# Kernel tuning notes

Measured on AMD Instinct MI355X. Metric: run time of the kernel, lower is better.

The kernel has to match this reference:

```python
import jax, jax.numpy as jnp
import numpy as np
from jax import lax

OUT = 24
THRESHOLD = 0.7
IOU_THRESHOLD = 0.5


def _conv(x, w, b):
    # x: [N,C,H,W], w: [O,I,kh,kw] (torch OIHW), valid padding, stride 1
    y = lax.conv_general_dilated(x, w, (1, 1), 'VALID',
                                 dimension_numbers=('NCHW', 'OIHW', 'NCHW'))
    return y + b[None, :, None, None]


def _prelu(x, a):
    a = a.reshape((1, -1) + (1,) * (x.ndim - 2))
    return jnp.where(x > 0, x, a * x)


def _maxpool(x, k, s, p):
    return lax.reduce_window(x, -jnp.inf, lax.max,
                             (1, 1, k, k), (1, 1, s, s),
                             [(0, 0), (0, 0), (p, p), (p, p)])


def _crop_resize(img, bboxes):
    # img: [3,H,W]; nearest-neighbor resize of each (clipped) crop to 24x24,
    # matching F.interpolate default nearest mode: src = floor(dst*in/out).
    _, H, W = img.shape
    x1 = jnp.clip(bboxes[:, 0].astype(jnp.int32), 0, W)
    y1 = jnp.clip(bboxes[:, 1].astype(jnp.int32), 0, H)
    x2 = jnp.clip(bboxes[:, 2].astype(jnp.int32), 0, W)
    y2 = jnp.clip(bboxes[:, 3].astype(jnp.int32), 0, H)
    j = jnp.arange(OUT)
    ix = jnp.clip(x1[:, None] + (j[None, :] * (x2 - x1)[:, None]) // OUT, 0, W - 1)  # [N,24]
    iy = jnp.clip(y1[:, None] + (j[None, :] * (y2 - y1)[:, None]) // OUT, 0, H - 1)  # [N,24]
    crops = img[:, iy[:, :, None], ix[:, None, :]]  # [3,N,24,24]
    return jnp.transpose(crops, (1, 0, 2, 3))        # [N,3,24,24]


def _pairwise_iou(b):
    x1 = jnp.maximum(b[:, None, 0], b[None, :, 0])
    y1 = jnp.maximum(b[:, None, 1], b[None, :, 1])
    x2 = jnp.minimum(b[:, None, 2], b[None, :, 2])
    y2 = jnp.minimum(b[:, None, 3], b[None, :, 3])
    inter = jnp.clip(x2 - x1, 0) * jnp.clip(y2 - y1, 0)
    area = jnp.clip(b[:, 2] - b[:, 0], 0) * jnp.clip(b[:, 3] - b[:, 1], 0)
    return inter / jnp.maximum(area[:, None] + area[None, :] - inter, 1e-12)


def _nms_keep(boxes, scores, valid, iou_thr):
    # Fixed-shape greedy NMS: returns boolean keep mask over original order.
    N = boxes.shape[0]
    order = jnp.argsort(-scores)
    b = boxes[order]
    v = valid[order]
    iou = _pairwise_iou(b)
    idx = jnp.arange(N)

    def body(i, supp):
        alive = v[i] & jnp.logical_not(supp[i])
        kill = alive & (iou[i] > iou_thr) & (idx > i)
        return supp | kill

    supp = lax.fori_loop(0, N, body, jnp.zeros((N,), bool))
    keep_sorted = v & jnp.logical_not(supp)
    return jnp.zeros((N,), bool).at[order].set(keep_sorted)


def _forward(image, bboxes, conv1_w, conv1_b, prelu1_a, conv2_w, conv2_b, prelu2_a,
             conv3_w, conv3_b, prelu3_a, lin4_w, lin4_b, prelu4_a,
             lin5a_w, lin5a_b, lin5b_w, lin5b_b):
    img = jnp.transpose((image - 127.5) * 0.0078125, (2, 0, 1))  # preprocess, HWC->CHW
    x = _crop_resize(img, bboxes)                                 # [N,3,24,24]
    x = _maxpool(_prelu(_conv(x, conv1_w, conv1_b), prelu1_a), 3, 2, 1)   # [N,28,11,11]
    x = _maxpool(_prelu(_conv(x, conv2_w, conv2_b), prelu2_a), 3, 2, 0)   # [N,48,4,4]
    x = _prelu(_conv(x, conv3_w, conv3_b), prelu3_a)                      # [N,64,3,3]
    x = x.reshape(x.shape[0], -1)                                          # [N,576]
    x = _prelu(x @ lin4_w.T + lin4_b, prelu4_a)                            # [N,128]
    cls = jax.nn.softmax(x @ lin5a_w.T + lin5a_b, axis=1)
    reg = x @ lin5b_w.T + lin5b_b
    scores = cls[:, 1]
    w = bboxes[:, 2] - bboxes[:, 0]
    h = bboxes[:, 3] - bboxes[:, 1]
    boxes = jnp.stack([bboxes[:, 0] + reg[:, 0] * w,
                       bboxes[:, 1] + reg[:, 1] * h,
                       bboxes[:, 2] + reg[:, 2] * w,
                       bboxes[:, 3] + reg[:, 3] * h], axis=1)
    return boxes, scores


def setup_inputs() -> dict:
    key = jax.random.key(0)
    ks = jax.random.split(key, 20)
    H, W, N = 1080, 1920, 4096
    image = jax.random.uniform(ks[0], (H, W, 3), jnp.float32, 0.0, 255.0)
    x1 = jax.random.randint(ks[1], (N,), 0, W - 96).astype(jnp.float32)
    y1 = jax.random.randint(ks[2], (N,), 0, H - 96).astype(jnp.float32)
    bw = jax.random.randint(ks[3], (N,), 24, 96).astype(jnp.float32)
    bh = jax.random.randint(ks[4], (N,), 24, 96).astype(jnp.float32)
    bboxes = jnp.stack([x1, y1, x1 + bw, y1 + bh], axis=1)

    def w(k, shape, scale):
        return jax.random.normal(k, shape, jnp.float32) * scale

    return dict(
        image=image, bboxes=bboxes,
        conv1_w=w(ks[5], (28, 3, 3, 3), 0.1), conv1_b=w(ks[6], (28,), 0.01),
        prelu1_a=jnp.full((28,), 0.25, jnp.float32),
        conv2_w=w(ks[7], (48, 28, 3, 3), 0.06), conv2_b=w(ks[8], (48,), 0.01),
        prelu2_a=jnp.full((48,), 0.25, jnp.float32),
        conv3_w=w(ks[9], (64, 48, 2, 2), 0.07), conv3_b=w(ks[10], (64,), 0.01),
        prelu3_a=jnp.full((64,), 0.25, jnp.float32),
        lin4_w=w(ks[11], (128, 576), 0.04), lin4_b=w(ks[12], (128,), 0.01),
        prelu4_a=jnp.full((128,), 0.25, jnp.float32),
        lin5a_w=w(ks[13], (2, 128), 0.2), lin5a_b=w(ks[14], (2,), 0.01),
        lin5b_w=w(ks[15], (4, 128), 0.09), lin5b_b=w(ks[16], (4,), 0.01),
    )


def reference(image, bboxes, conv1_w, conv1_b, prelu1_a, conv2_w, conv2_b, prelu2_a,
              conv3_w, conv3_b, prelu3_a, lin4_w, lin4_b, prelu4_a,
              lin5a_w, lin5a_b, lin5b_w, lin5b_b):
    boxes, scores = _forward(image, bboxes, conv1_w, conv1_b, prelu1_a,
                             conv2_w, conv2_b, prelu2_a, conv3_w, conv3_b, prelu3_a,
                             lin4_w, lin4_b, prelu4_a, lin5a_w, lin5a_b, lin5b_w, lin5b_b)
    valid = scores >= THRESHOLD
    keep = _nms_keep(boxes, scores, valid, IOU_THRESHOLD)
    # padded (masked) form of `bboxes[pick, :]` so output shape is static
    return jnp.where(keep[:, None], boxes, 0.0)
```

## Files before the change

kernel.cpp:

```cpp
#include <hip/hip_runtime.h>

typedef unsigned long long ull;
typedef __attribute__((ext_vector_type(8))) short bf16x8;
typedef __attribute__((ext_vector_type(4))) float f32x4;

#define W_IMG 1920
#define H_IMG 1080
#define NBOX 4096

#define S_CROP   0
#define S_CBUF   2016
#define S_PLANES 5152
#define S_BUF2   0
#define S_POOL2  3888
#define S_FEAT   0
#define S_VEC    576
#define S_LOUT   704
#define SMEM_F   8848

#define WS_BT    2277392
#define WS_BT1   2332688

__device__ __forceinline__ float4 ld4(const float* p) { return *(const float4*)p; }
__device__ __forceinline__ float prelu_f(float v, float a) { return v > 0.f ? v : a * v; }
__device__ __forceinline__ unsigned short bf16rn(float v) {
  unsigned u = __float_as_uint(v);
  return (unsigned short)((u + 0x7fffu + ((u >> 16) & 1u)) >> 16);
}
__device__ __forceinline__ float bf16tof(unsigned short h) {
  return __uint_as_float(((unsigned)h) << 16);
}

__global__ __launch_bounds__(256) void wconv_kernel(const float* __restrict__ w2,
                                                    const float* __restrict__ w1,
                                                    unsigned short* __restrict__ bt,
                                                    unsigned short* __restrict__ bt1) {
  int b = blockIdx.x, tid = threadIdx.x;
  if (b < 16) {
    for (int e = b*864 + tid; e < (b+1)*864; e += 256) {
      int c = e & 31, rest = e >> 5;
      int co = rest % 48, kk = rest / 48;
      float v = (c < 28) ? w2[co*252 + c*9 + kk] : 0.f;
      unsigned short h1 = bf16rn(v);
      bt[e] = h1;
      bt[13824 + e] = bf16rn(v - bf16tof(h1));
    }
  } else {
    for (int e = tid; e < 2048; e += 256) {
      int j = e & 7, rest = e >> 3;
      int co = rest & 31, pg = rest >> 5;
      int grp = pg & 3, plane = pg >> 2;
      int k = grp*8 + j;
      float v = (k < 27 && co < 28) ? w1[co*27 + k] : 0.f;
      unsigned short h1 = bf16rn(v);
      bt1[e] = plane ? bf16rn(v - bf16tof(h1)) : h1;
    }
  }
}

__global__ __launch_bounds__(256, 4) void cnn_kernel(
    const float* __restrict__ image, const float* __restrict__ bboxes,
    const unsigned short* __restrict__ wbt1,
    const float* __restrict__ b1, const float* __restrict__ a1,
    const unsigned short* __restrict__ wbt,
    const float* __restrict__ b2, const float* __restrict__ a2,
    const float* __restrict__ w3, const float* __restrict__ b3, const float* __restrict__ a3,
    const float* __restrict__ w4, const float* __restrict__ b4, const float* __restrict__ a4,
    const float* __restrict__ w5a, const float* __restrict__ b5a,
    const float* __restrict__ w5b, const float* __restrict__ b5b,
    float* __restrict__ boxes, float* __restrict__ scores)
{
  __shared__ float sm[SMEM_F];
  __shared__ int s_ix[24], s_iy[24];
  const int tid = threadIdx.x;
  const int n = blockIdx.x;
  const float lo = -__builtin_inff();
  const int lane = tid & 63, wv = tid >> 6;
  const int grp = lane >> 4, lr = lane & 15;

  bf16x8 c1B[2][2];
  {
    const bf16x8* btc = (const bf16x8*)wbt1;
    c1B[0][0] = btc[(0*4 + grp)*32 + lr];
    c1B[0][1] = btc[(0*4 + grp)*32 + 16 + lr];
    c1B[1][0] = btc[(1*4 + grp)*32 + lr];
    c1B[1][1] = btc[(1*4 + grp)*32 + 16 + lr];
  }
  int aoff[8];
#pragma unroll
  for (int j = 0; j < 8; ++j) {
    int k = grp*8 + j;
    int c = k / 9, rr = k - 9*c, ky = rr / 3, kx = rr - 3*ky;
    aoff[j] = c*672 + ky*28 + kx;
  }

  if (tid < 24) {
    int x1 = min(max((int)bboxes[n*4+0], 0), W_IMG);
    int x2 = min(max((int)bboxes[n*4+2], 0), W_IMG);
    s_ix[tid] = min(max(x1 + (tid*(x2-x1))/24, 0), W_IMG-1);
  } else if (tid >= 64 && tid < 88) {
    int j = tid - 64;
    int y1 = min(max((int)bboxes[n*4+1], 0), H_IMG);
    int y2 = min(max((int)bboxes[n*4+3], 0), H_IMG);
    s_iy[j] = min(max(y1 + (j*(y2-y1))/24, 0), H_IMG-1);
  }
  __syncthreads();
  for (int e = tid; e < 1728; e += 256) {
    int c = e / 576, rr = e % 576, y = rr / 24, x = rr % 24;
    float v = image[(s_iy[y]*W_IMG + s_ix[x])*3 + c];
    sm[S_CROP + c*672 + y*28 + x] = (v - 127.5f) * 0.0078125f;
  }
  __syncthreads();

  {
    unsigned short* cb = (unsigned short*)(sm + S_CBUF);
    unsigned short* pl = (unsigned short*)(sm + S_PLANES);
    const int c_r0[3] = {0, 7, 15};
    const int c_R [3] = {8, 9, 7};
    const int c_p0[3] = {0, 4, 8};
    const int c_np[3] = {4, 4, 3};
#pragma unroll 1
    for (int ck = 0; ck < 3; ++ck) {
      const int r0 = c_r0[ck], R = c_R[ck], p0 = c_p0[ck], np = c_np[ck];
      const int npix = R*22;
      const int mt = (npix + 15) >> 4;
#pragma unroll 1
      for (int t = wv; t < mt; t += 4) {
        int row = t*16 + lr;
        int pix = min(row, npix - 1);
        int ly = pix / 22;
        int x  = pix - ly*22;
        int base = (r0 + ly)*28 + x;
        unsigned short h1[8], h2[8];
#pragma unroll
        for (int j = 0; j < 8; ++j) {
          float v = 0.f;
          if (grp*8 + j < 27) v = sm[base + aoff[j]];
          h1[j] = bf16rn(v);
          h2[j] = bf16rn(v - bf16tof(h1[j]));
        }
        union { bf16x8 v; unsigned u[4]; } A1, A2;
#pragma unroll
        for (int q = 0; q < 4; ++q) {
          A1.u[q] = (unsigned)h1[2*q] | ((unsigned)h1[2*q+1] << 16);
          A2.u[q] = (unsigned)h2[2*q] | ((unsigned)h2[2*q+1] << 16);
        }
        f32x4 acc0 = {0.f,0.f,0.f,0.f}, acc1 = {0.f,0.f,0.f,0.f};
        acc0 = __builtin_amdgcn_mfma_f32_16x16x32_bf16(A1.v, c1B[1][0], acc0, 0, 0, 0);
        acc0 = __builtin_amdgcn_mfma_f32_16x16x32_bf16(A2.v, c1B[0][0], acc0, 0, 0, 0);
        acc0 = __builtin_amdgcn_mfma_f32_16x16x32_bf16(A1.v, c1B[0][0], acc0, 0, 0, 0);
        acc1 = __builtin_amdgcn_mfma_f32_16x16x32_bf16(A1.v, c1B[1][1], acc1, 0, 0, 0);
        acc1 = __builtin_amdgcn_mfma_f32_16x16x32_bf16(A2.v, c1B[0][1], acc1, 0, 0, 0);
        acc1 = __builtin_amdgcn_mfma_f32_16x16x32_bf16(A1.v, c1B[0][1], acc1, 0, 0, 0);
        int p0r = t*16 + grp*4;
        union { ull d; unsigned short s[4]; } W;
#pragma unroll
        for (int r = 0; r < 4; ++r) W.s[r] = bf16rn(acc0[r]);
        *(ull*)(cb + lr*224 + p0r) = W.d;
        if (lr < 12) {
#pragma unroll
          for (int r = 0; r < 4; ++r) W.s[r] = bf16rn(acc1[r]);
          *(ull*)(cb + (16 + lr)*224 + p0r) = W.d;
        }
      }
      __syncthreads();
      const int npt = np * 308;
      for (int o = tid; o < npt; o += 256) {
        int pyl = o / 308, rem = o - pyl*308;
        int co = rem / 11, px = rem - co*11;
        int py = p0 + pyl;
        int rlo = max(2*py - 1, 0) - r0, rhi = 2*py + 1 - r0;
        int clo = max(2*px - 1, 0), chi = min(2*px + 1, 21);
        float m = lo;
        for (int r = rlo; r <= rhi; ++r)
          for (int c2 = clo; c2 <= chi; ++c2)
            m = fmaxf(m, bf16tof(cb[co*224 + r*22 + c2]));
        float v = prelu_f(m + b1[co], a1[co]);
        unsigned short g1 = bf16rn(v);
        int it = (py*12 + px)*28 + co;
        pl[it] = g1;
        pl[3696 + it] = bf16rn(v - bf16tof(g1));
      }
      __syncthreads();
    }
  }

  {
    const unsigned short* pl = (const unsigned short*)(sm + S_PLANES);
    const bf16x8* bt = (const bf16x8*)wbt;
#pragma unroll 1
    for (int t = wv; t < 18; t += 4) {
      const int mtile = t / 3, ntile = t - 3*(t/3);
      const int co = ntile*16 + lr;
      const int arow = min(mtile*16 + lr, 80);
      const int oy = (arow*57) >> 9;
      const int ox = arow - 9*oy;
      const int pixb = (oy*12 + ox)*28 + grp*8;
      f32x4 acc = {0.f, 0.f, 0.f, 0.f};
#pragma unroll
      for (int kk = 0; kk < 9; ++kk) {
        const int ky = kk / 3, kx = kk - 3*(kk/3);
        const int aoff2 = pixb + (ky*12 + kx)*28;
        union { bf16x8 v; ull d[2]; } A1, A2;
        A1.d[0] = *(const ull*)(pl + aoff2);
        A1.d[1] = *(const ull*)(pl + aoff2 + 4);
        A2.d[0] = *(const ull*)(pl + 3696 + aoff2);
        A2.d[1] = *(const ull*)(pl + 3696 + aoff2 + 4);
        const bf16x8 B1 = bt[(kk*48 + co)*4 + grp];
        const bf16x8 B2 = bt[1728 + (kk*48 + co)*4 + grp];
        acc = __builtin_amdgcn_mfma_f32_16x16x32_bf16(A1.v, B2, acc, 0, 0, 0);
        acc = __builtin_amdgcn_mfma_f32_16x16x32_bf16(A2.v, B1, acc, 0, 0, 0);
        acc = __builtin_amdgcn_mfma_f32_16x16x32_bf16(A1.v, B1, acc, 0, 0, 0);
      }
      const float bb = b2[co], aa = a2[co];
      const int p0 = mtile*16 + grp*4;
#pragma unroll
      for (int r = 0; r < 4; ++r) {
        int p = p0 + r;
        if (p < 81) sm[S_BUF2 + co*81 + p] = prelu_f(acc[r] + bb, aa);
      }
    }
  }
  __syncthreads();

  for (int o = tid; o < 768; o += 256) {
    int cl = o >> 4, rem = o & 15, pyy = rem >> 2, pxx = rem & 3;
    float m = lo;
#pragma unroll
    for (int ky = 0; ky < 3; ++ky)
#pragma unroll
      for (int kx = 0; kx < 3; ++kx)
        m = fmaxf(m, sm[S_BUF2 + cl*81 + (2*pyy+ky)*9 + (2*pxx+kx)]);
    sm[S_POOL2 + o] = m;
  }
  __syncthreads();

  {
    int co = tid >> 2, c4 = tid & 3;
    float acc[9] = {};
    for (int cc = 0; cc < 12; ++cc) {
      int c = c4*12 + cc;
      float r[16];
      *(float4*)&r[0]  = ld4(sm + S_POOL2 + c*16);
      *(float4*)&r[4]  = ld4(sm + S_POOL2 + c*16 + 4);
      *(float4*)&r[8]  = ld4(sm + S_POOL2 + c*16 + 8);
      *(float4*)&r[12] = ld4(sm + S_POOL2 + c*16 + 12);
      float4 wq = ld4(&w3[co*192 + c*4]);
#pragma unroll
      for (int p = 0; p < 9; ++p) {
        int pyy = p / 3, pxx = p % 3;
        acc[p] += r[pyy*4+pxx]*wq.x + r[pyy*4+pxx+1]*wq.y
                + r[(pyy+1)*4+pxx]*wq.z + r[(pyy+1)*4+pxx+1]*wq.w;
      }
    }
#pragma unroll
    for (int p = 0; p < 9; ++p) {
      acc[p] += __shfl_xor(acc[p], 1, 64);
      acc[p] += __shfl_xor(acc[p], 2, 64);
    }
    if (c4 == 0) {
      float bb = b3[co], aa = a3[co];
#pragma unroll
      for (int p = 0; p < 9; ++p) sm[S_FEAT + co*9 + p] = prelu_f(acc[p] + bb, aa);
    }
  }
  __syncthreads();

  {
    for (int f = wv; f < 128; f += 4) {
      const float* wr = w4 + f*576;
      float acc = 0.f;
#pragma unroll
      for (int i = 0; i < 9; ++i) {
        int j = i*64 + lane;
        acc += wr[j] * sm[S_FEAT + j];
      }
#pragma unroll
      for (int off = 1; off < 64; off <<= 1) acc += __shfl_xor(acc, off, 64);
      if (lane == 0) sm[S_VEC + f] = prelu_f(acc + b4[f], a4[f]);
    }
  }
  __syncthreads();

  if (tid < 6) {
    const float* wr = (tid < 2) ? (w5a + tid*128) : (w5b + (tid-2)*128);
    float acc = 0.f;
#pragma unroll
    for (int j = 0; j < 32; ++j) {
      float4 xv = ld4(sm + S_VEC + j*4);
      float4 wv = ld4(wr + j*4);
      acc += xv.x*wv.x + xv.y*wv.y + xv.z*wv.z + xv.w*wv.w;
    }
    acc += (tid < 2) ? b5a[tid] : b5b[tid-2];
    sm[S_LOUT + tid] = acc;
  }
  __syncthreads();
  if (tid == 0) {
    float l0 = sm[S_LOUT+0], l1 = sm[S_LOUT+1];
    float m = fmaxf(l0, l1);
    float e0 = expf(l0 - m), e1 = expf(l1 - m);
    float sc = e1 / (e0 + e1);
    float4 bb = ld4(&bboxes[n*4]);
    float bw = bb.z - bb.x, bh = bb.w - bb.y;
    float4 ob = make_float4(bb.x + sm[S_LOUT+2]*bw, bb.y + sm[S_LOUT+3]*bh,
                            bb.z + sm[S_LOUT+4]*bw, bb.w + sm[S_LOUT+5]*bh);
    *(float4*)&boxes[n*4] = ob;
    scores[n] = sc;
  }
}

__global__ __launch_bounds__(1024) void sort_kernel(const float* __restrict__ scores,
                                                    const float* __restrict__ boxes,
                                                    int* __restrict__ order,
                                                    float* __restrict__ sboxes,
                                                    int* __restrict__ Vp) {
  __shared__ ull keys[NBOX];
  __shared__ int cnt;
  int tid = threadIdx.x;
  if (tid == 0) cnt = 0;
  __syncthreads();
  int local = 0;
  for (int i = tid; i < NBOX; i += 1024) {
    float s = scores[i];
    bool valid = (s >= 0.7f);
    unsigned hi = valid ? (0xFFFFFFFFu - __float_as_uint(s)) : 0xFFFFFFFFu;
    keys[i] = ((ull)hi << 32) | (unsigned)i;
    if (valid) local++;
  }
  atomicAdd(&cnt, local);
  __syncthreads();
  if (tid == 0) *Vp = cnt;
  if (cnt == 0) return;
  for (int k = 2; k <= NBOX; k <<= 1) {
    for (int j = k >> 1; j > 0; j >>= 1) {
      __syncthreads();
      for (int i = tid; i < NBOX; i += 1024) {
        int ij = i ^ j;
        if (ij > i) {
          ull a = keys[i], b = keys[ij];
          bool up = ((i & k) == 0);
          if ((a > b) == up) { keys[i] = b; keys[ij] = a; }
        }
      }
    }
  }
  __syncthreads();
  for (int i = tid; i < NBOX; i += 1024) {
    int idx = (int)(unsigned)(keys[i] & 0xFFFFFFFFu);
    order[i] = idx;
    *(float4*)&sboxes[i*4] = *(const float4*)&boxes[idx*4];
  }
}

__global__ __launch_bounds__(256) void iou_kernel(const float* __restrict__ sboxes,
                                                  const int* __restrict__ Vp,
                                                  ull* __restrict__ mask) {
  int i = blockIdx.x;
  int V = *Vp;
  if (i >= V) return;
  float4 bi = *(const float4*)&sboxes[i*4];
  float ai = fmaxf(bi.z - bi.x, 0.f) * fmaxf(bi.w - bi.y, 0.f);
  int lane = threadIdx.x & 63;
  for (int w = threadIdx.x >> 6; w < 64; w += 4) {
    int j = (w << 6) | lane;
    bool pred = false;
    if (j > i && j < V) {
      float4 bj = *(const float4*)&sboxes[j*4];
      float aj = fmaxf(bj.z - bj.x, 0.f) * fmaxf(bj.w - bj.y, 0.f);
      float xx1 = fmaxf(bi.x, bj.x), yy1 = fmaxf(bi.y, bj.y);
      float xx2 = fminf(bi.z, bj.z), yy2 = fminf(bi.w, bj.w);
      float inter = fmaxf(xx2 - xx1, 0.f) * fmaxf(yy2 - yy1, 0.f);
      float den = fmaxf(ai + aj - inter, 1e-12f);
      pred = (inter / den) > 0.5f;
    }
    ull bits = __ballot(pred);
    if (lane == 0) mask[(size_t)i*64 + w] = bits;
  }
}

#define CHUNK 16
__global__ __launch_bounds__(64) void nms_scan(const ull* __restrict__ mask,
                                               const int* __restrict__ Vp,
                                               const int* __restrict__ order,
                                               int* __restrict__ keep) {
  int lane = threadIdx.x;
  for (int idx = lane; idx < NBOX; idx += 64) keep[idx] = 0;
  __syncthreads();
  int V = *Vp;
  ull remw = 0;
  __shared__ ull buf[CHUNK][64];
  for (int base = 0; base < V; base += CHUNK) {
    int nn = min(CHUNK, V - base);
#pragma unroll
    for (int r = 0; r < CHUNK; ++r)
      if (r < nn) buf[r][lane] = mask[(size_t)(base + r)*64 + lane];
    for (int r = 0; r < nn; ++r) {
      int i = base + r;
      ull w = __shfl(remw, i >> 6, 64);
      if (!((w >> (i & 63)) & 1ull)) {
        remw |= buf[r][lane];
        if (lane == 0) keep[order[i]] = 1;
      }
    }
  }
}

__global__ __launch_bounds__(256) void out_kernel(const float* __restrict__ boxes,
                                                  const int* __restrict__ keep,
                                                  float* __restrict__ out) {
  int n = blockIdx.x * 256 + threadIdx.x;
  float4 b = *(const float4*)&boxes[n*4];
  float4 z = make_float4(0.f, 0.f, 0.f, 0.f);
  *(float4*)&out[n*4] = keep[n] ? b : z;
}

extern "C" void kernel_launch(void* const* d_in, const int* in_sizes, int n_in,
                              void* d_out, int out_size, void* d_ws, size_t ws_size,
                              hipStream_t stream) {
  const float* image  = (const float*)d_in[0];
  const float* bboxes = (const float*)d_in[1];
  const float* w1  = (const float*)d_in[2];
  const float* b1  = (const float*)d_in[3];
  const float* a1  = (const float*)d_in[4];
  const float* w2  = (const float*)d_in[5];
  const float* b2  = (const float*)d_in[6];
  const float* a2  = (const float*)d_in[7];
  const float* w3  = (const float*)d_in[8];
  const float* b3  = (const float*)d_in[9];
  const float* a3  = (const float*)d_in[10];
  const float* w4  = (const float*)d_in[11];
  const float* b4  = (const float*)d_in[12];
  const float* a4  = (const float*)d_in[13];
  const float* w5a = (const float*)d_in[14];
  const float* b5a = (const float*)d_in[15];
  const float* w5b = (const float*)d_in[16];
  const float* b5b = (const float*)d_in[17];

  char* ws = (char*)d_ws;
  float* boxes  = (float*)(ws + 0);
  float* scores = (float*)(ws + 65536);
  float* sboxes = (float*)(ws + 81920);
  int*   order  = (int*)  (ws + 147456);
  int*   Vp     = (int*)  (ws + 163840);
  int*   keep   = (int*)  (ws + 163856);
  ull*   mask   = (ull*)  (ws + 180240);
  unsigned short* wbt  = (unsigned short*)(ws + WS_BT);
  unsigned short* wbt1 = (unsigned short*)(ws + WS_BT1);

  float* out = (float*)d_out;

  wconv_kernel<<<17, 256, 0, stream>>>(w2, w1, wbt, wbt1);
  cnn_kernel<<<NBOX, 256, 0, stream>>>(image, bboxes, wbt1, b1,a1, wbt, b2,a2, w3,b3,a3,
                                       w4,b4,a4, w5a,b5a, w5b,b5b, boxes, scores);
  sort_kernel<<<1, 1024, 0, stream>>>(scores, boxes, order, sboxes, Vp);
  iou_kernel<<<NBOX, 256, 0, stream>>>(sboxes, Vp, mask);
  nms_scan<<<1, 64, 0, stream>>>(mask, Vp, order, keep);
  out_kernel<<<16, 256, 0, stream>>>(boxes, keep, out);
}
```

Baseline: 399.0 us.

## Drop split-bf16 error compensation in conv1/conv2 and fuse NMS scan with output

Conv1 and conv2 previously used a hi/lo bf16 split of weights and activations, issuing three MFMAs per product to approximate fp32 accuracy. They now use a single bf16 plane and one MFMA each, and the crop is stored as bf16 in shared memory. This roughly cuts matrix work and shared-memory footprint, allowing a higher occupancy hint of 6 blocks per SM. The NMS scan and output kernels are merged to save a launch, and the conv buffer stride is padded. The lower precision risks flipping threshold or IoU decisions against the reference.

```diff
diff --git a/kernel.cpp b/kernel.cpp
--- a/kernel.cpp
+++ b/kernel.cpp
@@ -8,18 +8,18 @@
 #define H_IMG 1080
 #define NBOX 4096
 
-#define S_CROP   0
-#define S_CBUF   2016
-#define S_PLANES 5152
+#define S_CROP_SH 0
+#define S_CBUF_SH 2016
+#define S_PLANE_SH 8400
 #define S_BUF2   0
 #define S_POOL2  3888
 #define S_FEAT   0
 #define S_VEC    576
 #define S_LOUT   704
-#define SMEM_F   8848
+#define SMEM_F   6048
 
 #define WS_BT    2277392
-#define WS_BT1   2332688
+#define WS_BT1   2305040
 
 __device__ __forceinline__ float4 ld4(const float* p) { return *(const float4*)p; }
 __device__ __forceinline__ float prelu_f(float v, float a) { return v > 0.f ? v : a * v; }
@@ -41,24 +41,20 @@
       int c = e & 31, rest = e >> 5;
       int co = rest % 48, kk = rest / 48;
       float v = (c < 28) ? w2[co*252 + c*9 + kk] : 0.f;
-      unsigned short h1 = bf16rn(v);
-      bt[e] = h1;
-      bt[13824 + e] = bf16rn(v - bf16tof(h1));
+      bt[e] = bf16rn(v);
     }
   } else {
-    for (int e = tid; e < 2048; e += 256) {
+    for (int e = tid; e < 1024; e += 256) {
       int j = e & 7, rest = e >> 3;
-      int co = rest & 31, pg = rest >> 5;
-      int grp = pg & 3, plane = pg >> 2;
+      int co = rest & 31, grp = rest >> 5;
       int k = grp*8 + j;
       float v = (k < 27 && co < 28) ? w1[co*27 + k] : 0.f;
-      unsigned short h1 = bf16rn(v);
-      bt1[e] = plane ? bf16rn(v - bf16tof(h1)) : h1;
-    }
-  }
-}
-
-__global__ __launch_bounds__(256, 4) void cnn_kernel(
+      bt1[e] = bf16rn(v);
+    }
+  }
+}
+
+__global__ __launch_bounds__(256, 6) void cnn_kernel(
     const float* __restrict__ image, const float* __restrict__ bboxes,
     const unsigned short* __restrict__ wbt1,
     const float* __restrict__ b1, const float* __restrict__ a1,
@@ -77,14 +73,13 @@
   const float lo = -__builtin_inff();
   const int lane = tid & 63, wv = tid >> 6;
   const int grp = lane >> 4, lr = lane & 15;
-
-  bf16x8 c1B[2][2];
+  unsigned short* csh = (unsigned short*)sm;
+
+  bf16x8 c1B[2];
   {
     const bf16x8* btc = (const bf16x8*)wbt1;
-    c1B[0][0] = btc[(0*4 + grp)*32 + lr];
-    c1B[0][1] = btc[(0*4 + grp)*32 + 16 + lr];
-    c1B[1][0] = btc[(1*4 + grp)*32 + lr];
-    c1B[1][1] = btc[(1*4 + grp)*32 + 16 + lr];
+    c1B[0] = btc[grp*32 + lr];
+    c1B[1] = btc[grp*32 + 16 + lr];
   }
   int aoff[8];
 #pragma unroll
@@ -108,13 +103,13 @@
   for (int e = tid; e < 1728; e += 256) {
     int c = e / 576, rr = e % 576, y = rr / 24, x = rr % 24;
     float v = image[(s_iy[y]*W_IMG + s_ix[x])*3 + c];
-    sm[S_CROP + c*672 + y*28 + x] = (v - 127.5f) * 0.0078125f;
+    csh[S_CROP_SH + c*672 + y*28 + x] = bf16rn((v - 127.5f) * 0.0078125f);
   }
   __syncthreads();
 
   {
-    unsigned short* cb = (unsigned short*)(sm + S_CBUF);
-    unsigned short* pl = (unsigned short*)(sm + S_PLANES);
+    unsigned short* cb = csh + S_CBUF_SH;
+    unsigned short* pl = csh + S_PLANE_SH;
     const int c_r0[3] = {0, 7, 15};
     const int c_R [3] = {8, 9, 7};
     const int c_p0[3] = {0, 4, 8};
@@ -131,36 +126,26 @@
         int ly = pix / 22;
         int x  = pix - ly*22;
         int base = (r0 + ly)*28 + x;
-        unsigned short h1[8], h2[8];
-#pragma unroll
-        for (int j = 0; j < 8; ++j) {
-          float v = 0.f;
-          if (grp*8 + j < 27) v = sm[base + aoff[j]];
-          h1[j] = bf16rn(v);
-          h2[j] = bf16rn(v - bf16tof(h1[j]));
-        }
-        union { bf16x8 v; unsigned u[4]; } A1, A2;
-#pragma unroll
-        for (int q = 0; q < 4; ++q) {
+        unsigned short h1[8];
+#pragma unroll
+        for (int j = 0; j < 8; ++j)
+          h1[j] = (grp*8 + j < 27) ? csh[base + aoff[j]] : (unsigned short)0;
+        union { bf16x8 v; unsigned u[4]; } A1;
+#pragma unroll
+        for (int q = 0; q < 4; ++q)
           A1.u[q] = (unsigned)h1[2*q] | ((unsigned)h1[2*q+1] << 16);
-          A2.u[q] = (unsigned)h2[2*q] | ((unsigned)h2[2*q+1] << 16);
-        }
         f32x4 acc0 = {0.f,0.f,0.f,0.f}, acc1 = {0.f,0.f,0.f,0.f};
-        acc0 = __builtin_amdgcn_mfma_f32_16x16x32_bf16(A1.v, c1B[1][0], acc0, 0, 0, 0);
-        acc0 = __builtin_amdgcn_mfma_f32_16x16x32_bf16(A2.v, c1B[0][0], acc0, 0, 0, 0);
-        acc0 = __builtin_amdgcn_mfma_f32_16x16x32_bf16(A1.v, c1B[0][0], acc0, 0, 0, 0);
-        acc1 = __builtin_amdgcn_mfma_f32_16x16x32_bf16(A1.v, c1B[1][1], acc1, 0, 0, 0);
-        acc1 = __builtin_amdgcn_mfma_f32_16x16x32_bf16(A2.v, c1B[0][1], acc1, 0, 0, 0);
-        acc1 = __builtin_amdgcn_mfma_f32_16x16x32_bf16(A1.v, c1B[0][1], acc1, 0, 0, 0);
+        acc0 = __builtin_amdgcn_mfma_f32_16x16x32_bf16(A1.v, c1B[0], acc0, 0, 0, 0);
+        acc1 = __builtin_amdgcn_mfma_f32_16x16x32_bf16(A1.v, c1B[1], acc1, 0, 0, 0);
         int p0r = t*16 + grp*4;
         union { ull d; unsigned short s[4]; } W;
 #pragma unroll
         for (int r = 0; r < 4; ++r) W.s[r] = bf16rn(acc0[r]);
-        *(ull*)(cb + lr*224 + p0r) = W.d;
+        *(ull*)(cb + lr*228 + p0r) = W.d;
         if (lr < 12) {
 #pragma unroll
           for (int r = 0; r < 4; ++r) W.s[r] = bf16rn(acc1[r]);
-          *(ull*)(cb + (16 + lr)*224 + p0r) = W.d;
+          *(ull*)(cb + (16 + lr)*228 + p0r) = W.d;
         }
       }
       __syncthreads();
@@ -174,19 +159,16 @@
         float m = lo;
         for (int r = rlo; r <= rhi; ++r)
           for (int c2 = clo; c2 <= chi; ++c2)
-            m = fmaxf(m, bf16tof(cb[co*224 + r*22 + c2]));
+            m = fmaxf(m, bf16tof(cb[co*228 + r*22 + c2]));
         float v = prelu_f(m + b1[co], a1[co]);
-        unsigned short g1 = bf16rn(v);
-        int it = (py*12 + px)*28 + co;
-        pl[it] = g1;
-        pl[3696 + it] = bf16rn(v - bf16tof(g1));
+        pl[(py*12 + px)*28 + co] = bf16rn(v);
       }
       __syncthreads();
     }
   }
 
   {
-    const unsigned short* pl = (const unsigned short*)(sm + S_PLANES);
+    const unsigned short* pl = csh + S_PLANE_SH;
     const bf16x8* bt = (const bf16x8*)wbt;
 #pragma unroll 1
     for (int t = wv; t < 18; t += 4) {
@@ -201,15 +183,10 @@
       for (int kk = 0; kk < 9; ++kk) {
         const int ky = kk / 3, kx = kk - 3*(kk/3);
         const int aoff2 = pixb + (ky*12 + kx)*28;
-        union { bf16x8 v; ull d[2]; } A1, A2;
+        union { bf16x8 v; ull d[2]; } A1;
         A1.d[0] = *(const ull*)(pl + aoff2);
         A1.d[1] = *(const ull*)(pl + aoff2 + 4);
-        A2.d[0] = *(const ull*)(pl + 3696 + aoff2);
-        A2.d[1] = *(const ull*)(pl + 3696 + aoff2 + 4);
         const bf16x8 B1 = bt[(kk*48 + co)*4 + grp];
-        const bf16x8 B2 = bt[1728 + (kk*48 + co)*4 + grp];
-        acc = __builtin_amdgcn_mfma_f32_16x16x32_bf16(A1.v, B2, acc, 0, 0, 0);
-        acc = __builtin_amdgcn_mfma_f32_16x16x32_bf16(A2.v, B1, acc, 0, 0, 0);
         acc = __builtin_amdgcn_mfma_f32_16x16x32_bf16(A1.v, B1, acc, 0, 0, 0);
       }
       const float bb = b2[co], aa = a2[co];
@@ -379,16 +356,21 @@
 }
 
 #define CHUNK 16
-__global__ __launch_bounds__(64) void nms_scan(const ull* __restrict__ mask,
-                                               const int* __restrict__ Vp,
-                                               const int* __restrict__ order,
-                                               int* __restrict__ keep) {
+__global__ __launch_bounds__(64) void nms_out(const ull* __restrict__ mask,
+                                              const int* __restrict__ Vp,
+                                              const int* __restrict__ order,
+                                              const float* __restrict__ boxes,
+                                              float* __restrict__ out) {
+  __shared__ ull buf[CHUNK][64];
+  __shared__ int klist[NBOX];
+  __shared__ int kc;
   int lane = threadIdx.x;
-  for (int idx = lane; idx < NBOX; idx += 64) keep[idx] = 0;
+  if (lane == 0) kc = 0;
+  float4 z = make_float4(0.f, 0.f, 0.f, 0.f);
+  for (int i = lane; i < NBOX; i += 64) *(float4*)&out[i*4] = z;
   __syncthreads();
   int V = *Vp;
   ull remw = 0;
-  __shared__ ull buf[CHUNK][64];
   for (int base = 0; base < V; base += CHUNK) {
     int nn = min(CHUNK, V - base);
 #pragma unroll
@@ -399,19 +381,15 @@
       ull w = __shfl(remw, i >> 6, 64);
       if (!((w >> (i & 63)) & 1ull)) {
         remw |= buf[r][lane];
-        if (lane == 0) keep[order[i]] = 1;
-      }
-    }
-  }
-}
-
-__global__ __launch_bounds__(256) void out_kernel(const float* __restrict__ boxes,
-                                                  const int* __restrict__ keep,
-                                                  float* __restrict__ out) {
-  int n = blockIdx.x * 256 + threadIdx.x;
-  float4 b = *(const float4*)&boxes[n*4];
-  float4 z = make_float4(0.f, 0.f, 0.f, 0.f);
-  *(float4*)&out[n*4] = keep[n] ? b : z;
+        if (lane == 0) klist[kc++] = order[i];
+      }
+    }
+  }
+  __syncthreads();
+  for (int j = lane; j < kc; j += 64) {
+    int oi = klist[j];
+    *(float4*)&out[oi*4] = *(const float4*)&boxes[oi*4];
+  }
 }
 
 extern "C" void kernel_launch(void* const* d_in, const int* in_sizes, int n_in,
@@ -442,7 +420,6 @@
   float* sboxes = (float*)(ws + 81920);
   int*   order  = (int*)  (ws + 147456);
   int*   Vp     = (int*)  (ws + 163840);
-  int*   keep   = (int*)  (ws + 163856);
   ull*   mask   = (ull*)  (ws + 180240);
   unsigned short* wbt  = (unsigned short*)(ws + WS_BT);
   unsigned short* wbt1 = (unsigned short*)(ws + WS_BT1);
@@ -454,6 +431,5 @@
                                        w4,b4,a4, w5a,b5a, w5b,b5b, boxes, scores);
   sort_kernel<<<1, 1024, 0, stream>>>(scores, boxes, order, sboxes, Vp);
   iou_kernel<<<NBOX, 256, 0, stream>>>(sboxes, Vp, mask);
-  nms_scan<<<1, 64, 0, stream>>>(mask, Vp, order, keep);
-  out_kernel<<<16, 256, 0, stream>>>(boxes, keep, out);
-}
+  nms_out<<<1, 64, 0, stream>>>(mask, Vp, order, boxes, out);
+}
```

Result: faster. 342.5 us (-14.1%).
